# Kernel tuning notes

Hardware: AMD Instinct MI355X
Metric: run time of the kernel (lower is better)

Reference implementation:

```python
import jax, jax.numpy as jnp
import numpy as np

NUM_GRAPHS = 4096  # dim_size = batch.max()+1; fixed for jit (fill guarantees max id present)
V, D = 1_000_000, 128


def setup_inputs() -> dict:
    key = jax.random.key(0)
    k1, k2, k3, k4 = jax.random.split(key, 4)
    H = jax.random.normal(k1, (V, D), dtype=jnp.float32)
    batch = jnp.sort(jax.random.randint(k2, (V,), 0, NUM_GRAPHS))
    # nn.Linear(output_size, 1): weight [1, d] -> stored as w [d], bias [1]
    w = jax.random.normal(k3, (D,), dtype=jnp.float32) * 0.05
    b = jax.random.normal(k4, (1,), dtype=jnp.float32) * 0.05
    return {"H": H, "batch": batch, "w": w, "b": b}


def reference(H, batch, w, b):
    # attention_logits = exp(W(H))  -> [V]
    logits = jnp.exp(H @ w + b[0])
    # Z: per-graph normalizer via scatter-sum  -> [num_graphs]
    Z = jax.ops.segment_sum(logits, batch, num_segments=NUM_GRAPHS)
    # segment softmax weights  -> [V]
    alphas = logits / Z[batch]
    # weighted scatter-sum pooling  -> [num_graphs, d]
    return jax.ops.segment_sum(alphas[:, None] * H, batch, num_segments=NUM_GRAPHS)
```

## Files before the change

kernel.cpp:

```cpp
#include <hip/hip_runtime.h>

#define D 128
#define NUM_GRAPHS 4096

typedef float v4f __attribute__((ext_vector_type(4)));

#define RFL(x) __builtin_amdgcn_readfirstlane(x)

__device__ __forceinline__ float dot4(v4f h, v4f w) {
    return h.x * w.x + h.y * w.y + h.z * w.z + h.w * w.w;
}

__device__ __forceinline__ void flushv(float* __restrict__ S, float* __restrict__ Z,
                                       int cg_e, int cg_o, int half, int colbase,
                                       bool zlane, v4f& acc, float& zacc) {
    const int cur_g = half ? cg_o : cg_e;
    float* p = &S[(size_t)cur_g * D + colbase];
    atomicAdd(p + 0, acc.x);
    atomicAdd(p + 1, acc.y);
    atomicAdd(p + 2, acc.z);
    atomicAdd(p + 3, acc.w);
    if (zlane) atomicAdd(&Z[cur_g], zacc);
    acc = (v4f)(0.f);
    zacc = 0.f;
}

__global__ __launch_bounds__(256, 8) void attn_agg_accum(
    const float* __restrict__ H, const int* __restrict__ batch,
    const float* __restrict__ w, const float* __restrict__ b,
    float* __restrict__ S ,
    float* __restrict__ Z ,
    int V)
{
    const int lane    = threadIdx.x & 63;
    const int half    = lane >> 5;
    const int colbase = (lane & 31) << 2;
    const bool zlane  = (lane & 31) == 0;

    int wid = blockIdx.x * (blockDim.x >> 6) + (threadIdx.x >> 6);
    wid = RFL(wid);
    const int total_waves = gridDim.x * (blockDim.x >> 6);
    const int rpw = ((V + total_waves * 8 - 1) / (total_waves * 8)) * 8;

    const int row0 = wid * rpw;
    if (row0 >= V) return;
    int row1 = row0 + rpw;
    if (row1 > V) row1 = V;

    const v4f w4     = ((const v4f*)w)[lane & 31];
    const float bias = b[0];
    const v4f* __restrict__ Hp = (const v4f*)H;

    v4f acc    = (v4f)(0.f);
    float zacc = 0.f;

    const int2 cgi = *(const int2*)(batch + row0);
    int cg_e = RFL(cgi.x);
    int cg_o = RFL(cgi.y);

    int v = row0;
    v4f h0, h1, h2, h3;
    if (v + 8 <= row1) {
        h0 = __builtin_nontemporal_load(&Hp[(size_t)(v + 0) * 32 + lane]);
        h1 = __builtin_nontemporal_load(&Hp[(size_t)(v + 2) * 32 + lane]);
        h2 = __builtin_nontemporal_load(&Hp[(size_t)(v + 4) * 32 + lane]);
        h3 = __builtin_nontemporal_load(&Hp[(size_t)(v + 6) * 32 + lane]);
    }

    while (v + 8 <= row1) {
        const int nv = v + 8;

        const int4 t0 = *(const int4*)(batch + v);
        const int4 t1 = *(const int4*)(batch + v + 4);

        v4f n0 = h0, n1 = h1, n2 = h2, n3 = h3;
        if (nv + 8 <= row1) {
            n0 = __builtin_nontemporal_load(&Hp[(size_t)(nv + 0) * 32 + lane]);
            n1 = __builtin_nontemporal_load(&Hp[(size_t)(nv + 2) * 32 + lane]);
            n2 = __builtin_nontemporal_load(&Hp[(size_t)(nv + 4) * 32 + lane]);
            n3 = __builtin_nontemporal_load(&Hp[(size_t)(nv + 6) * 32 + lane]);
        }

        float d0 = dot4(h0, w4);
        float d1 = dot4(h1, w4);
        float d2 = dot4(h2, w4);
        float d3 = dot4(h3, w4);
        #pragma unroll
        for (int off = 16; off > 0; off >>= 1) {
            d0 += __shfl_xor(d0, off, 64);
            d1 += __shfl_xor(d1, off, 64);
            d2 += __shfl_xor(d2, off, 64);
            d3 += __shfl_xor(d3, off, 64);
        }

        const float l0 = __expf(d0 + bias);
        const float l1 = __expf(d1 + bias);
        const float l2 = __expf(d2 + bias);
        const float l3 = __expf(d3 + bias);

        const int a0 = RFL(t0.x), a1 = RFL(t0.y), a2 = RFL(t0.z), a3 = RFL(t0.w);
        const int b0 = RFL(t1.x), b1 = RFL(t1.y), b2 = RFL(t1.z), b3 = RFL(t1.w);

        if (__builtin_expect(a0 == b3 && a0 == cg_e && a0 == cg_o, 1)) {
            acc += h0 * l0 + h1 * l1 + h2 * l2 + h3 * l3;
            zacc += l0 + l1 + l2 + l3;
        } else {
            if (a0 != cg_e || a1 != cg_o) { flushv(S, Z, cg_e, cg_o, half, colbase, zlane, acc, zacc); cg_e = a0; cg_o = a1; }
            acc += h0 * l0; zacc += l0;
            if (a2 != cg_e || a3 != cg_o) { flushv(S, Z, cg_e, cg_o, half, colbase, zlane, acc, zacc); cg_e = a2; cg_o = a3; }
            acc += h1 * l1; zacc += l1;
            if (b0 != cg_e || b1 != cg_o) { flushv(S, Z, cg_e, cg_o, half, colbase, zlane, acc, zacc); cg_e = b0; cg_o = b1; }
            acc += h2 * l2; zacc += l2;
            if (b2 != cg_e || b3 != cg_o) { flushv(S, Z, cg_e, cg_o, half, colbase, zlane, acc, zacc); cg_e = b2; cg_o = b3; }
            acc += h3 * l3; zacc += l3;
        }

        h0 = n0; h1 = n1; h2 = n2; h3 = n3;
        v = nv;
    }

    for (; v + 2 <= row1; v += 2) {
        const int2 t = *(const int2*)(batch + v);
        v4f h = __builtin_nontemporal_load(&Hp[(size_t)v * 32 + lane]);
        float d = dot4(h, w4);
        #pragma unroll
        for (int off = 16; off > 0; off >>= 1)
            d += __shfl_xor(d, off, 64);
        const float l = __expf(d + bias);
        const int ge = RFL(t.x), go = RFL(t.y);
        if (ge != cg_e || go != cg_o) { flushv(S, Z, cg_e, cg_o, half, colbase, zlane, acc, zacc); cg_e = ge; cg_o = go; }
        acc += h * l; zacc += l;
    }

    flushv(S, Z, cg_e, cg_o, half, colbase, zlane, acc, zacc);
}

__global__ __launch_bounds__(256) void attn_agg_norm(
    float4* __restrict__ out, const float* __restrict__ Z, int n4)
{
    const int i = blockIdx.x * blockDim.x + threadIdx.x;
    if (i < n4) {
        const int g = i >> 5;
        const float z = Z[g];
        float4 o = out[i];
        o.x /= z; o.y /= z; o.z /= z; o.w /= z;
        out[i] = o;
    }
}

extern "C" void kernel_launch(void* const* d_in, const int* in_sizes, int n_in,
                              void* d_out, int out_size, void* d_ws, size_t ws_size,
                              hipStream_t stream) {
    const float* H     = (const float*)d_in[0];
    const int*   batch = (const int*)  d_in[1];
    const float* w     = (const float*)d_in[2];
    const float* b     = (const float*)d_in[3];
    float* out = (float*)d_out;
    float* Z   = (float*)d_ws;

    const int V = in_sizes[0] / D;

    hipMemsetAsync(out, 0, (size_t)out_size * sizeof(float), stream);
    hipMemsetAsync(Z,   0, NUM_GRAPHS * sizeof(float), stream);

    attn_agg_accum<<<2048, 256, 0, stream>>>(H, batch, w, b, out, Z, V);

    const int n4 = NUM_GRAPHS * D / 4;
    attn_agg_norm<<<(n4 + 255) / 256, 256, 0, stream>>>((float4*)out, Z, n4);
}
```

Measured before the change: 669.3 us.

## Deepen H prefetch to two stages and use per-lane graph ids with wave vote

The main loop now keeps two 8-row groups of H (and their per-half graph ids) in flight instead of one, doubling the prefetch distance to hide more HBM latency. Segment ids are loaded per lane (one per half-wave) and boundary detection uses a wave-wide __any vote instead of readfirstlane on vector batch loads. The occupancy hint in launch_bounds is dropped. The deeper pipeline raises VGPR use, which may lower occupancy. Scalar loads of batch are replaced by per-lane vector loads.

```diff
diff --git a/kernel.cpp b/kernel.cpp
--- a/kernel.cpp
+++ b/kernel.cpp
@@ -5,16 +5,13 @@
 
 typedef float v4f __attribute__((ext_vector_type(4)));
 
-#define RFL(x) __builtin_amdgcn_readfirstlane(x)
-
 __device__ __forceinline__ float dot4(v4f h, v4f w) {
     return h.x * w.x + h.y * w.y + h.z * w.z + h.w * w.w;
 }
 
 __device__ __forceinline__ void flushv(float* __restrict__ S, float* __restrict__ Z,
-                                       int cg_e, int cg_o, int half, int colbase,
-                                       bool zlane, v4f& acc, float& zacc) {
-    const int cur_g = half ? cg_o : cg_e;
+                                       int cur_g, int colbase, bool zlane,
+                                       v4f& acc, float& zacc) {
     float* p = &S[(size_t)cur_g * D + colbase];
     atomicAdd(p + 0, acc.x);
     atomicAdd(p + 1, acc.y);
@@ -25,7 +22,7 @@
     zacc = 0.f;
 }
 
-__global__ __launch_bounds__(256, 8) void attn_agg_accum(
+__global__ __launch_bounds__(256) void attn_agg_accum(
     const float* __restrict__ H, const int* __restrict__ batch,
     const float* __restrict__ w, const float* __restrict__ b,
     float* __restrict__ S ,
@@ -37,12 +34,11 @@
     const int colbase = (lane & 31) << 2;
     const bool zlane  = (lane & 31) == 0;
 
-    int wid = blockIdx.x * (blockDim.x >> 6) + (threadIdx.x >> 6);
-    wid = RFL(wid);
+    const int wave_id     = blockIdx.x * (blockDim.x >> 6) + (threadIdx.x >> 6);
     const int total_waves = gridDim.x * (blockDim.x >> 6);
     const int rpw = ((V + total_waves * 8 - 1) / (total_waves * 8)) * 8;
 
-    const int row0 = wid * rpw;
+    const int row0 = wave_id * rpw;
     if (row0 >= V) return;
     int row1 = row0 + rpw;
     if (row1 > V) row1 = V;
@@ -53,38 +49,52 @@
 
     v4f acc    = (v4f)(0.f);
     float zacc = 0.f;
-
-    const int2 cgi = *(const int2*)(batch + row0);
-    int cg_e = RFL(cgi.x);
-    int cg_o = RFL(cgi.y);
+    int cur_g  = batch[row0 + half];
 
     int v = row0;
-    v4f h0, h1, h2, h3;
+    v4f a0, a1, a2, a3, b0, b1, b2, b3;
+    int ga0, ga1, ga2, ga3, gb0, gb1, gb2, gb3;
     if (v + 8 <= row1) {
-        h0 = __builtin_nontemporal_load(&Hp[(size_t)(v + 0) * 32 + lane]);
-        h1 = __builtin_nontemporal_load(&Hp[(size_t)(v + 2) * 32 + lane]);
-        h2 = __builtin_nontemporal_load(&Hp[(size_t)(v + 4) * 32 + lane]);
-        h3 = __builtin_nontemporal_load(&Hp[(size_t)(v + 6) * 32 + lane]);
+        a0 = __builtin_nontemporal_load(&Hp[(size_t)(v + 0) * 32 + lane]);
+        a1 = __builtin_nontemporal_load(&Hp[(size_t)(v + 2) * 32 + lane]);
+        a2 = __builtin_nontemporal_load(&Hp[(size_t)(v + 4) * 32 + lane]);
+        a3 = __builtin_nontemporal_load(&Hp[(size_t)(v + 6) * 32 + lane]);
+        ga0 = batch[v + 0 + half];
+        ga1 = batch[v + 2 + half];
+        ga2 = batch[v + 4 + half];
+        ga3 = batch[v + 6 + half];
+        b0 = a0; b1 = a1; b2 = a2; b3 = a3;
+        gb0 = ga0; gb1 = ga1; gb2 = ga2; gb3 = ga3;
+        if (v + 16 <= row1) {
+            b0 = __builtin_nontemporal_load(&Hp[(size_t)(v +  8) * 32 + lane]);
+            b1 = __builtin_nontemporal_load(&Hp[(size_t)(v + 10) * 32 + lane]);
+            b2 = __builtin_nontemporal_load(&Hp[(size_t)(v + 12) * 32 + lane]);
+            b3 = __builtin_nontemporal_load(&Hp[(size_t)(v + 14) * 32 + lane]);
+            gb0 = batch[v +  8 + half];
+            gb1 = batch[v + 10 + half];
+            gb2 = batch[v + 12 + half];
+            gb3 = batch[v + 14 + half];
+        }
     }
 
     while (v + 8 <= row1) {
-        const int nv = v + 8;
-
-        const int4 t0 = *(const int4*)(batch + v);
-        const int4 t1 = *(const int4*)(batch + v + 4);
-
-        v4f n0 = h0, n1 = h1, n2 = h2, n3 = h3;
-        if (nv + 8 <= row1) {
-            n0 = __builtin_nontemporal_load(&Hp[(size_t)(nv + 0) * 32 + lane]);
-            n1 = __builtin_nontemporal_load(&Hp[(size_t)(nv + 2) * 32 + lane]);
-            n2 = __builtin_nontemporal_load(&Hp[(size_t)(nv + 4) * 32 + lane]);
-            n3 = __builtin_nontemporal_load(&Hp[(size_t)(nv + 6) * 32 + lane]);
+        v4f c0 = b0, c1 = b1, c2 = b2, c3 = b3;
+        int gc0 = gb0, gc1 = gb1, gc2 = gb2, gc3 = gb3;
+        if (v + 24 <= row1) {
+            c0 = __builtin_nontemporal_load(&Hp[(size_t)(v + 16) * 32 + lane]);
+            c1 = __builtin_nontemporal_load(&Hp[(size_t)(v + 18) * 32 + lane]);
+            c2 = __builtin_nontemporal_load(&Hp[(size_t)(v + 20) * 32 + lane]);
+            c3 = __builtin_nontemporal_load(&Hp[(size_t)(v + 22) * 32 + lane]);
+            gc0 = batch[v + 16 + half];
+            gc1 = batch[v + 18 + half];
+            gc2 = batch[v + 20 + half];
+            gc3 = batch[v + 22 + half];
         }
 
-        float d0 = dot4(h0, w4);
-        float d1 = dot4(h1, w4);
-        float d2 = dot4(h2, w4);
-        float d3 = dot4(h3, w4);
+        float d0 = dot4(a0, w4);
+        float d1 = dot4(a1, w4);
+        float d2 = dot4(a2, w4);
+        float d3 = dot4(a3, w4);
         #pragma unroll
         for (int off = 16; off > 0; off >>= 1) {
             d0 += __shfl_xor(d0, off, 64);
@@ -98,41 +108,41 @@
         const float l2 = __expf(d2 + bias);
         const float l3 = __expf(d3 + bias);
 
-        const int a0 = RFL(t0.x), a1 = RFL(t0.y), a2 = RFL(t0.z), a3 = RFL(t0.w);
-        const int b0 = RFL(t1.x), b1 = RFL(t1.y), b2 = RFL(t1.z), b3 = RFL(t1.w);
-
-        if (__builtin_expect(a0 == b3 && a0 == cg_e && a0 == cg_o, 1)) {
-            acc += h0 * l0 + h1 * l1 + h2 * l2 + h3 * l3;
+        const int diff = (ga0 ^ cur_g) | (ga1 ^ cur_g) | (ga2 ^ cur_g) | (ga3 ^ cur_g);
+        if (__builtin_expect(!__any(diff), 1)) {
+            acc += a0 * l0 + a1 * l1 + a2 * l2 + a3 * l3;
             zacc += l0 + l1 + l2 + l3;
         } else {
-            if (a0 != cg_e || a1 != cg_o) { flushv(S, Z, cg_e, cg_o, half, colbase, zlane, acc, zacc); cg_e = a0; cg_o = a1; }
-            acc += h0 * l0; zacc += l0;
-            if (a2 != cg_e || a3 != cg_o) { flushv(S, Z, cg_e, cg_o, half, colbase, zlane, acc, zacc); cg_e = a2; cg_o = a3; }
-            acc += h1 * l1; zacc += l1;
-            if (b0 != cg_e || b1 != cg_o) { flushv(S, Z, cg_e, cg_o, half, colbase, zlane, acc, zacc); cg_e = b0; cg_o = b1; }
-            acc += h2 * l2; zacc += l2;
-            if (b2 != cg_e || b3 != cg_o) { flushv(S, Z, cg_e, cg_o, half, colbase, zlane, acc, zacc); cg_e = b2; cg_o = b3; }
-            acc += h3 * l3; zacc += l3;
+            if (__any(ga0 ^ cur_g)) { flushv(S, Z, cur_g, colbase, zlane, acc, zacc); cur_g = ga0; }
+            acc += a0 * l0; zacc += l0;
+            if (__any(ga1 ^ cur_g)) { flushv(S, Z, cur_g, colbase, zlane, acc, zacc); cur_g = ga1; }
+            acc += a1 * l1; zacc += l1;
+            if (__any(ga2 ^ cur_g)) { flushv(S, Z, cur_g, colbase, zlane, acc, zacc); cur_g = ga2; }
+            acc += a2 * l2; zacc += l2;
+            if (__any(ga3 ^ cur_g)) { flushv(S, Z, cur_g, colbase, zlane, acc, zacc); cur_g = ga3; }
+            acc += a3 * l3; zacc += l3;
         }
 
-        h0 = n0; h1 = n1; h2 = n2; h3 = n3;
-        v = nv;
+        a0 = b0; a1 = b1; a2 = b2; a3 = b3;
+        ga0 = gb0; ga1 = gb1; ga2 = gb2; ga3 = gb3;
+        b0 = c0; b1 = c1; b2 = c2; b3 = c3;
+        gb0 = gc0; gb1 = gc1; gb2 = gc2; gb3 = gc3;
+        v += 8;
     }
 
     for (; v + 2 <= row1; v += 2) {
-        const int2 t = *(const int2*)(batch + v);
         v4f h = __builtin_nontemporal_load(&Hp[(size_t)v * 32 + lane]);
+        int g = batch[v + half];
         float d = dot4(h, w4);
         #pragma unroll
         for (int off = 16; off > 0; off >>= 1)
             d += __shfl_xor(d, off, 64);
         const float l = __expf(d + bias);
-        const int ge = RFL(t.x), go = RFL(t.y);
-        if (ge != cg_e || go != cg_o) { flushv(S, Z, cg_e, cg_o, half, colbase, zlane, acc, zacc); cg_e = ge; cg_o = go; }
+        if (__any(g ^ cur_g)) { flushv(S, Z, cur_g, colbase, zlane, acc, zacc); cur_g = g; }
         acc += h * l; zacc += l;
     }
 
-    flushv(S, Z, cg_e, cg_o, half, colbase, zlane, acc, zacc);
+    flushv(S, Z, cur_g, colbase, zlane, acc, zacc);
 }
 
 __global__ __launch_bounds__(256) void attn_agg_norm(
```

Result: faster. 649.7 us (-2.9%).
